# Kernel optimization log

Hardware: AMD Instinct MI355X
Metric: run time of the kernel (lower is better)

## Reference

```python
import jax, jax.numpy as jnp
import numpy as np

NEG_INF = -jnp.inf

def _sage_conv(x_src, x_dst, src, dst, Wl, bl, Wr, aggr, num_nodes):
    # messages = source features gathered along edges  [E, d]
    msgs = x_src[src]
    if aggr == 'mean':
        s = jax.ops.segment_sum(msgs, dst, num_segments=num_nodes)
        cnt = jax.ops.segment_sum(jnp.ones((src.shape[0],), x_src.dtype), dst, num_segments=num_nodes)
        agg = s / jnp.maximum(cnt, 1.0)[:, None]
    else:  # max; isolated targets -> 0 (PyG scatter-max fill)
        m = jax.ops.segment_max(msgs, dst, num_segments=num_nodes)
        agg = jnp.where(jnp.isfinite(m), m, 0.0)
    return agg @ Wl.T + bl + x_dst @ Wr.T

def setup_inputs() -> dict:
    key = jax.random.key(0)
    ks = jax.random.split(key, 12)
    N, E, D, H, C, L = 40000, 640000, 128, 128, 64, 2
    sc = 0.05
    return {
        'x': jax.random.normal(ks[0], (N, D), jnp.float32),
        'edge_index0': jax.random.randint(ks[1], (2, E), 0, N, jnp.int64),
        'edge_index1': jax.random.randint(ks[2], (2, E), 0, N, jnp.int64),
        'Wl_mean': jax.random.normal(ks[3], (L, H, D), jnp.float32) * sc,
        'bl_mean': jax.random.normal(ks[4], (L, H), jnp.float32) * sc,
        'Wr_mean': jax.random.normal(ks[5], (L, H, D), jnp.float32) * sc,
        'Wl_max': jax.random.normal(ks[6], (L, H, D), jnp.float32) * sc,
        'bl_max': jax.random.normal(ks[7], (L, H), jnp.float32) * sc,
        'Wr_max': jax.random.normal(ks[8], (L, H, D), jnp.float32) * sc,
        'post_W': jax.random.normal(ks[9], (C, 2 * L * H), jnp.float32) * sc,
        'post_b': jax.random.normal(ks[10], (C,), jnp.float32) * sc,
    }

def reference(x, edge_index0, edge_index1, Wl_mean, bl_mean, Wr_mean, Wl_max, bl_max, Wr_max, post_W, post_b):
    N = x.shape[0]
    edge_sets = [edge_index0, edge_index1]
    L = len(edge_sets)
    h = x
    all_layers = []
    for i, ei in enumerate(edge_sets):
        src, dst = ei[0], ei[1]
        x_mean = _sage_conv(h, h, src, dst, Wl_mean[i], bl_mean[i], Wr_mean[i], 'mean', N)
        x_max = _sage_conv(h, h, src, dst, Wl_max[i], bl_max[i], Wr_max[i], 'max', N)
        all_layers.append(x_mean)
        all_layers.append(x_max)
        if i != L - 1:
            h = jax.nn.relu(h)  # note: original never replaces x with conv output
    x_final = jnp.concatenate(all_layers, axis=1) @ post_W.T + post_b
    return jax.nn.log_softmax(x_final, axis=-1)
```

## Files before the change

### kernel.cpp

```cpp
#include <hip/hip_runtime.h>
#include <cstdint>
#include <cstddef>

constexpr int FD = 128;
constexpr int CC = 64;
constexpr int KTOT = 768;
constexpr int CAP = 48;
constexpr int EPT = 4;

typedef __attribute__((ext_vector_type(8))) short short8;
typedef __attribute__((ext_vector_type(4))) float f32x4;

__device__ __forceinline__ float bf2f(unsigned u16) {
  union { unsigned u; float f; } v; v.u = u16 << 16; return v.f;
}
__device__ __forceinline__ unsigned f2bf(float f) {
  union { float f; unsigned u; } v; v.f = f;
  return (v.u + 0x7FFFu + ((v.u >> 16) & 1u)) >> 16;
}
__device__ __forceinline__ unsigned pack2(float a, float b) {
  return f2bf(a) | (f2bf(b) << 16);
}
__device__ __forceinline__ unsigned relu_pk(unsigned v) {
  unsigned m = ((v >> 15) & 0x10001u) * 0xFFFFu;
  return v & ~m;
}

__global__ void init_kernel(const float* __restrict__ x, uint4* __restrict__ xbf4,
                            int n8, int* __restrict__ cnt, int ncnt) {
  int t = blockIdx.x * blockDim.x + threadIdx.x;
  if (t < ncnt) cnt[t] = 0;
  if (t >= n8) return;
  float4 a = *(const float4*)(x + (size_t)t * 8);
  float4 b = *(const float4*)(x + (size_t)t * 8 + 4);
  uint4 q;
  q.x = pack2(a.x, a.y); q.y = pack2(a.z, a.w);
  q.z = pack2(b.x, b.y); q.w = pack2(b.z, b.w);
  xbf4[t] = q;
}

__global__ void precompute_kernel(
    const float* __restrict__ Wl_mean, const float* __restrict__ bl_mean,
    const float* __restrict__ Wr_mean, const float* __restrict__ Wl_max,
    const float* __restrict__ bl_max,  const float* __restrict__ Wr_max,
    const float* __restrict__ postW,   const float* __restrict__ postb,
    unsigned short* __restrict__ Mbf, float* __restrict__ cb)
{
  int t = blockIdx.x * blockDim.x + threadIdx.x;
  if (t >= KTOT * CC) return;
  int c  = t & (CC - 1);
  int k  = t >> 6;
  int blk = k >> 7;
  int kk  = k & 127;
  const float* pw = postW + (size_t)c * 512;
  float acc = 0.f;
  if (blk < 4) {
    const float* W;
    if (blk == 0)      W = Wl_mean;
    else if (blk == 1) W = Wl_max;
    else if (blk == 2) W = Wl_mean + 128 * 128;
    else               W = Wl_max + 128 * 128;
    const float* p = pw + blk * 128;
    #pragma unroll 8
    for (int h = 0; h < 128; ++h) acc += p[h] * W[h * 128 + kk];
  } else if (blk == 4) {
    #pragma unroll 8
    for (int h = 0; h < 128; ++h)
      acc += pw[h] * Wr_mean[h * 128 + kk] + pw[128 + h] * Wr_max[h * 128 + kk];
  } else {
    const float* Wm = Wr_mean + 128 * 128;
    const float* Wx = Wr_max + 128 * 128;
    #pragma unroll 8
    for (int h = 0; h < 128; ++h)
      acc += pw[256 + h] * Wm[h * 128 + kk] + pw[384 + h] * Wx[h * 128 + kk];
  }
  Mbf[(size_t)c * KTOT + k] = (unsigned short)f2bf(acc);

  if (t < CC) {
    const float* pwc = postW + (size_t)t * 512;
    float b = postb[t];
    for (int h = 0; h < 128; ++h) {
      b += bl_mean[h]        * pwc[h]
         + bl_max[h]         * pwc[128 + h]
         + bl_mean[128 + h]  * pwc[256 + h]
         + bl_max[128 + h]   * pwc[384 + h];
    }
    cb[t] = b;
  }
}

__global__ __launch_bounds__(256) void build_kernel(
    const int* __restrict__ e0, int E0,
    const int* __restrict__ e1, int E1,
    int* __restrict__ cnt, unsigned short* __restrict__ csrf, int N)
{
  int t = blockIdx.x * blockDim.x + threadIdx.x;
  const int nt0 = (E0 + EPT - 1) / EPT;
  const int nt1 = (E1 + EPT - 1) / EPT;
  if (t >= nt0 + nt1) return;
  const int twoN = 2 * N;
  const int* e; int E; int cb2; int ti;
  if (t < nt0) { e = e0; E = E0; cb2 = 0; ti = t; }
  else         { e = e1; E = E1; cb2 = N; ti = t - nt0; }
  const int i0 = ti * EPT;

  if (i0 + EPT <= E) {
    int4 s4 = *(const int4*)(e + i0);
    int4 d4 = *(const int4*)(e + E + i0);
    int s[EPT] = {s4.x, s4.y, s4.z, s4.w};
    int d[EPT] = {d4.x, d4.y, d4.z, d4.w};
    int p[EPT];
    #pragma unroll
    for (int u = 0; u < EPT; ++u) p[u] = atomicAdd(&cnt[cb2 + d[u]], 1);
    #pragma unroll
    for (int u = 0; u < EPT; ++u)
      if (p[u] < CAP) csrf[(size_t)p[u] * twoN + cb2 + d[u]] = (unsigned short)s[u];
  } else {
    const int n = E - i0;
    for (int u = 0; u < n; ++u) {
      int ss = e[i0 + u], dd = e[E + i0 + u];
      int pp = atomicAdd(&cnt[cb2 + dd], 1);
      if (pp < CAP) csrf[(size_t)pp * twoN + cb2 + dd] = (unsigned short)ss;
    }
  }
}

__global__ __launch_bounds__(256) void agg_kernel(
    const unsigned* __restrict__ xbf, const int* __restrict__ cnt,
    const unsigned short* __restrict__ csrf, unsigned* __restrict__ aggbf, int N)
{
  int gw = (blockIdx.x * 256 + threadIdx.x) >> 6;
  int lane = threadIdx.x & 63;
  if (gw >= 2 * N) return;
  const int twoN = 2 * N;
  const int layer = (gw >= N) ? 1 : 0;
  const int node = gw - layer * N;
  const int deg = min(cnt[gw], CAP);
  const int half = lane >> 5;
  const int hl = lane & 31;
  const float lo = layer ? 0.f : -INFINITY;

  const int n0 = (deg + 1) >> 1;
  const int cbeg = half ? n0 : 0;
  const int ce = half ? deg : n0;

  float s0 = 0.f, s1 = 0.f, s2 = 0.f, s3 = 0.f;
  float m0 = -INFINITY, m1 = -INFINITY, m2 = -INFINITY, m3 = -INFINITY;

  for (int c = cbeg; c < ce; c += 8) {
    int idx[8];
    bool val[8];
    #pragma unroll
    for (int u = 0; u < 8; ++u) {
      int cc = c + u;
      val[u] = cc < ce;
      idx[u] = (int)csrf[(size_t)(val[u] ? cc : (ce - 1)) * twoN + gw];
    }
    uint2 g[8];
    #pragma unroll
    for (int u = 0; u < 8; ++u)
      g[u] = *(const uint2*)(xbf + (size_t)idx[u] * 64 + hl * 2);
    #pragma unroll
    for (int u = 0; u < 8; ++u) {
      float a0 = fmaxf(bf2f(g[u].x & 0xffffu), lo);
      float a1 = fmaxf(bf2f(g[u].x >> 16), lo);
      float a2 = fmaxf(bf2f(g[u].y & 0xffffu), lo);
      float a3 = fmaxf(bf2f(g[u].y >> 16), lo);
      s0 += val[u] ? a0 : 0.f;  s1 += val[u] ? a1 : 0.f;
      s2 += val[u] ? a2 : 0.f;  s3 += val[u] ? a3 : 0.f;
      m0 = fmaxf(m0, val[u] ? a0 : -INFINITY);
      m1 = fmaxf(m1, val[u] ? a1 : -INFINITY);
      m2 = fmaxf(m2, val[u] ? a2 : -INFINITY);
      m3 = fmaxf(m3, val[u] ? a3 : -INFINITY);
    }
  }

  s0 += __shfl_xor(s0, 32); s1 += __shfl_xor(s1, 32);
  s2 += __shfl_xor(s2, 32); s3 += __shfl_xor(s3, 32);
  m0 = fmaxf(m0, __shfl_xor(m0, 32)); m1 = fmaxf(m1, __shfl_xor(m1, 32));
  m2 = fmaxf(m2, __shfl_xor(m2, 32)); m3 = fmaxf(m3, __shfl_xor(m3, 32));

  if (half == 0) {
    float inv = 1.f / (float)(deg > 0 ? deg : 1);
    if (deg == 0) { m0 = 0.f; m1 = 0.f; m2 = 0.f; m3 = 0.f; }
    unsigned* am = aggbf + (size_t)(layer * 2)     * N * 64;
    unsigned* ax = aggbf + (size_t)(layer * 2 + 1) * N * 64;
    size_t o = (size_t)node * 64 + hl * 2;
    *(uint2*)(am + o) = make_uint2(pack2(s0 * inv, s1 * inv), pack2(s2 * inv, s3 * inv));
    *(uint2*)(ax + o) = make_uint2(pack2(m0, m1), pack2(m2, m3));
  }
}

__global__ __launch_bounds__(256) void gemm_kernel(
    const unsigned* __restrict__ aggbf, const unsigned* __restrict__ xbf,
    const unsigned short* __restrict__ Mbf, const float* __restrict__ cb,
    float* __restrict__ out, int N)
{
  const int tid = threadIdx.x;
  const int w = tid >> 6, l = tid & 63;
  const int l15 = l & 15, lg = l >> 4;
  const int rowb = blockIdx.x * 128 + w * 32;
  const int r0 = rowb + l15, r1 = r0 + 16;
  const size_t a0r = (size_t)min(r0, N - 1) * 64;
  const size_t a1r = (size_t)min(r1, N - 1) * 64;
  const int kg = lg * 8;
  const size_t N64 = (size_t)N * 64;

  f32x4 acc[2][4];
  #pragma unroll
  for (int i = 0; i < 2; ++i)
    #pragma unroll
    for (int j = 0; j < 4; ++j) acc[i][j] = (f32x4){0.f, 0.f, 0.f, 0.f};

  #pragma unroll
  for (int b6 = 0; b6 < 6; ++b6) {
    const unsigned* Ap = (b6 < 4) ? (aggbf + (size_t)b6 * N64) : xbf;
    #pragma unroll
    for (int ss = 0; ss < 4; ++ss) {
      const int k0 = b6 * 128 + ss * 32;
      const int ko = (ss * 32 + kg) >> 1;
      uint4 ua = *(const uint4*)(Ap + a0r + ko);
      uint4 ub = *(const uint4*)(Ap + a1r + ko);
      if (b6 == 5) {
        ua.x = relu_pk(ua.x); ua.y = relu_pk(ua.y);
        ua.z = relu_pk(ua.z); ua.w = relu_pk(ua.w);
        ub.x = relu_pk(ub.x); ub.y = relu_pk(ub.y);
        ub.z = relu_pk(ub.z); ub.w = relu_pk(ub.w);
      }
      short8 af0 = __builtin_bit_cast(short8, ua);
      short8 af1 = __builtin_bit_cast(short8, ub);
      #pragma unroll
      for (int fc = 0; fc < 4; ++fc) {
        const int c = fc * 16 + l15;
        uint4 qb = *(const uint4*)(Mbf + (size_t)c * KTOT + k0 + kg);
        short8 bf = __builtin_bit_cast(short8, qb);
        acc[0][fc] = __builtin_amdgcn_mfma_f32_16x16x32_bf16(af0, bf, acc[0][fc], 0, 0, 0);
        acc[1][fc] = __builtin_amdgcn_mfma_f32_16x16x32_bf16(af1, bf, acc[1][fc], 0, 0, 0);
      }
    }
  }

  float bias[4];
  #pragma unroll
  for (int fc = 0; fc < 4; ++fc) bias[fc] = cb[fc * 16 + l15];

  #pragma unroll
  for (int fr = 0; fr < 2; ++fr) {
    #pragma unroll
    for (int i = 0; i < 4; ++i) {
      int row = rowb + fr * 16 + lg * 4 + i;
      float z0 = acc[fr][0][i] + bias[0];
      float z1 = acc[fr][1][i] + bias[1];
      float z2 = acc[fr][2][i] + bias[2];
      float z3 = acc[fr][3][i] + bias[3];
      float m = fmaxf(fmaxf(z0, z1), fmaxf(z2, z3));
      #pragma unroll
      for (int o = 1; o < 16; o <<= 1) m = fmaxf(m, __shfl_xor(m, o));
      float s = expf(z0 - m) + expf(z1 - m) + expf(z2 - m) + expf(z3 - m);
      #pragma unroll
      for (int o = 1; o < 16; o <<= 1) s += __shfl_xor(s, o);
      float lse = m + logf(s);
      if (row < N) {
        size_t ob = (size_t)row * CC + l15;
        out[ob]      = z0 - lse;
        out[ob + 16] = z1 - lse;
        out[ob + 32] = z2 - lse;
        out[ob + 48] = z3 - lse;
      }
    }
  }
}

extern "C" void kernel_launch(void* const* d_in, const int* in_sizes, int n_in,
                              void* d_out, int out_size, void* d_ws, size_t ws_size,
                              hipStream_t stream)
{
  const float* x       = (const float*)d_in[0];
  const int*   e0      = (const int*)d_in[1];
  const int*   e1      = (const int*)d_in[2];
  const float* Wl_mean = (const float*)d_in[3];
  const float* bl_mean = (const float*)d_in[4];
  const float* Wr_mean = (const float*)d_in[5];
  const float* Wl_max  = (const float*)d_in[6];
  const float* bl_max  = (const float*)d_in[7];
  const float* Wr_max  = (const float*)d_in[8];
  const float* postW   = (const float*)d_in[9];
  const float* postb   = (const float*)d_in[10];
  float* out = (float*)d_out;

  const int N  = in_sizes[0] / FD;
  const int E0 = in_sizes[1] / 2;
  const int E1 = in_sizes[2] / 2;

  char* ws = (char*)d_ws;
  size_t off = 0;
  auto alloc = [&](size_t bytes) -> void* {
    void* p = ws + off;
    off = (off + bytes + 255) & ~(size_t)255;
    return p;
  };
  unsigned short* Mbf  = (unsigned short*)alloc((size_t)KTOT * CC * 2);
  float*          cbv  = (float*)alloc(CC * 4);
  int*            cnt  = (int*)alloc((size_t)2 * N * 4);
  unsigned short* csrf = (unsigned short*)alloc((size_t)2 * N * CAP * 2);
  unsigned*       xbf  = (unsigned*)alloc((size_t)N * 64 * 4);
  unsigned*       aggbf= (unsigned*)alloc((size_t)4 * N * 64 * 4);
  (void)ws_size; (void)n_in; (void)out_size;

  const int n8 = N * 16;
  init_kernel<<<dim3((n8 + 255) / 256), dim3(256), 0, stream>>>(
      x, (uint4*)xbf, n8, cnt, 2 * N);

  precompute_kernel<<<dim3((KTOT * CC + 255) / 256), dim3(256), 0, stream>>>(
      Wl_mean, bl_mean, Wr_mean, Wl_max, bl_max, Wr_max, postW, postb, Mbf, cbv);

  const int nthr = (E0 + EPT - 1) / EPT + (E1 + EPT - 1) / EPT;
  build_kernel<<<dim3((nthr + 255) / 256), dim3(256), 0, stream>>>(
      e0, E0, e1, E1, cnt, csrf, N);

  const int aggBlocks = (2 * N * 64 + 255) / 256;
  agg_kernel<<<dim3(aggBlocks), dim3(256), 0, stream>>>(xbf, cnt, csrf, aggbf, N);

  gemm_kernel<<<dim3((N + 127) / 128), dim3(256), 0, stream>>>(
      aggbf, xbf, Mbf, cbv, out, N);
}
```

Measured before the change: 277.6 us.

## Fuse all stages into one persistent cooperative kernel with grid syncs

Replaces the five separate launches (init, precompute, CSR build, aggregation, GEMM) with a single cooperative persistent kernel that runs grid-stride loops and uses grid.sync between phases. The GEMM phase also changes from 128-row tiles with two fragments per wave to 64-row tiles with one fragment per wave. The goal is to remove launch gaps and kernel-boundary overheads. The cost is grid-wide barriers, a grid capped by occupancy (at most 2048 blocks), less latency hiding in the gather-heavy aggregation, and possible register pressure from launch_bounds(256,4).

```diff
diff --git a/kernel.cpp b/kernel.cpp
--- a/kernel.cpp
+++ b/kernel.cpp
@@ -1,4 +1,5 @@
 #include <hip/hip_runtime.h>
+#include <hip/hip_cooperative_groups.h>
 #include <cstdint>
 #include <cstddef>
 
@@ -26,246 +27,246 @@
   return v & ~m;
 }
 
-__global__ void init_kernel(const float* __restrict__ x, uint4* __restrict__ xbf4,
-                            int n8, int* __restrict__ cnt, int ncnt) {
-  int t = blockIdx.x * blockDim.x + threadIdx.x;
-  if (t < ncnt) cnt[t] = 0;
-  if (t >= n8) return;
-  float4 a = *(const float4*)(x + (size_t)t * 8);
-  float4 b = *(const float4*)(x + (size_t)t * 8 + 4);
-  uint4 q;
-  q.x = pack2(a.x, a.y); q.y = pack2(a.z, a.w);
-  q.z = pack2(b.x, b.y); q.w = pack2(b.z, b.w);
-  xbf4[t] = q;
-}
-
-__global__ void precompute_kernel(
-    const float* __restrict__ Wl_mean, const float* __restrict__ bl_mean,
-    const float* __restrict__ Wr_mean, const float* __restrict__ Wl_max,
-    const float* __restrict__ bl_max,  const float* __restrict__ Wr_max,
-    const float* __restrict__ postW,   const float* __restrict__ postb,
-    unsigned short* __restrict__ Mbf, float* __restrict__ cb)
-{
-  int t = blockIdx.x * blockDim.x + threadIdx.x;
-  if (t >= KTOT * CC) return;
-  int c  = t & (CC - 1);
-  int k  = t >> 6;
-  int blk = k >> 7;
-  int kk  = k & 127;
-  const float* pw = postW + (size_t)c * 512;
-  float acc = 0.f;
-  if (blk < 4) {
-    const float* W;
-    if (blk == 0)      W = Wl_mean;
-    else if (blk == 1) W = Wl_max;
-    else if (blk == 2) W = Wl_mean + 128 * 128;
-    else               W = Wl_max + 128 * 128;
-    const float* p = pw + blk * 128;
-    #pragma unroll 8
-    for (int h = 0; h < 128; ++h) acc += p[h] * W[h * 128 + kk];
-  } else if (blk == 4) {
-    #pragma unroll 8
-    for (int h = 0; h < 128; ++h)
-      acc += pw[h] * Wr_mean[h * 128 + kk] + pw[128 + h] * Wr_max[h * 128 + kk];
-  } else {
-    const float* Wm = Wr_mean + 128 * 128;
-    const float* Wx = Wr_max + 128 * 128;
-    #pragma unroll 8
-    for (int h = 0; h < 128; ++h)
-      acc += pw[256 + h] * Wm[h * 128 + kk] + pw[384 + h] * Wx[h * 128 + kk];
-  }
-  Mbf[(size_t)c * KTOT + k] = (unsigned short)f2bf(acc);
-
-  if (t < CC) {
-    const float* pwc = postW + (size_t)t * 512;
-    float b = postb[t];
-    for (int h = 0; h < 128; ++h) {
-      b += bl_mean[h]        * pwc[h]
-         + bl_max[h]         * pwc[128 + h]
-         + bl_mean[128 + h]  * pwc[256 + h]
-         + bl_max[128 + h]   * pwc[384 + h];
-    }
-    cb[t] = b;
-  }
-}
-
-__global__ __launch_bounds__(256) void build_kernel(
-    const int* __restrict__ e0, int E0,
-    const int* __restrict__ e1, int E1,
-    int* __restrict__ cnt, unsigned short* __restrict__ csrf, int N)
-{
-  int t = blockIdx.x * blockDim.x + threadIdx.x;
-  const int nt0 = (E0 + EPT - 1) / EPT;
-  const int nt1 = (E1 + EPT - 1) / EPT;
-  if (t >= nt0 + nt1) return;
+struct MegaParams {
+  const float* x;
+  const int* e0;
+  const int* e1;
+  const float *Wl_mean, *bl_mean, *Wr_mean, *Wl_max, *bl_max, *Wr_max, *postW, *postb;
+  unsigned short* Mbf;
+  float* cb;
+  int* cnt;
+  unsigned short* csrf;
+  unsigned* xbf;
+  unsigned* aggbf;
+  float* out;
+  int N, E0, E1;
+};
+
+__global__ __launch_bounds__(256, 4) void mega_kernel(MegaParams p) {
+  cooperative_groups::grid_group grid = cooperative_groups::this_grid();
+  const int tid = threadIdx.x;
+  const int gtid = blockIdx.x * 256 + tid;
+  const int gsz = gridDim.x * 256;
+  const int N = p.N;
   const int twoN = 2 * N;
-  const int* e; int E; int cb2; int ti;
-  if (t < nt0) { e = e0; E = E0; cb2 = 0; ti = t; }
-  else         { e = e1; E = E1; cb2 = N; ti = t - nt0; }
-  const int i0 = ti * EPT;
-
-  if (i0 + EPT <= E) {
-    int4 s4 = *(const int4*)(e + i0);
-    int4 d4 = *(const int4*)(e + E + i0);
-    int s[EPT] = {s4.x, s4.y, s4.z, s4.w};
-    int d[EPT] = {d4.x, d4.y, d4.z, d4.w};
-    int p[EPT];
+
+  for (int t = gtid; t < twoN; t += gsz) p.cnt[t] = 0;
+
+  const int n8 = N * 16;
+  for (int t = gtid; t < n8; t += gsz) {
+    float4 a = *(const float4*)(p.x + (size_t)t * 8);
+    float4 b = *(const float4*)(p.x + (size_t)t * 8 + 4);
+    uint4 q;
+    q.x = pack2(a.x, a.y); q.y = pack2(a.z, a.w);
+    q.z = pack2(b.x, b.y); q.w = pack2(b.z, b.w);
+    ((uint4*)p.xbf)[t] = q;
+  }
+
+  for (int t = gtid; t < KTOT * CC; t += gsz) {
+    int c  = t & (CC - 1);
+    int k  = t >> 6;
+    int blk = k >> 7;
+    int kk  = k & 127;
+    const float* pw = p.postW + (size_t)c * 512;
+    float acc = 0.f;
+    if (blk < 4) {
+      const float* W;
+      if (blk == 0)      W = p.Wl_mean;
+      else if (blk == 1) W = p.Wl_max;
+      else if (blk == 2) W = p.Wl_mean + 128 * 128;
+      else               W = p.Wl_max + 128 * 128;
+      const float* pp = pw + blk * 128;
+      #pragma unroll 8
+      for (int h = 0; h < 128; ++h) acc += pp[h] * W[h * 128 + kk];
+    } else if (blk == 4) {
+      #pragma unroll 8
+      for (int h = 0; h < 128; ++h)
+        acc += pw[h] * p.Wr_mean[h * 128 + kk] + pw[128 + h] * p.Wr_max[h * 128 + kk];
+    } else {
+      const float* Wm = p.Wr_mean + 128 * 128;
+      const float* Wx = p.Wr_max + 128 * 128;
+      #pragma unroll 8
+      for (int h = 0; h < 128; ++h)
+        acc += pw[256 + h] * Wm[h * 128 + kk] + pw[384 + h] * Wx[h * 128 + kk];
+    }
+    p.Mbf[(size_t)c * KTOT + k] = (unsigned short)f2bf(acc);
+
+    if (t < CC) {
+      const float* pwc = p.postW + (size_t)t * 512;
+      float b = p.postb[t];
+      for (int h = 0; h < 128; ++h) {
+        b += p.bl_mean[h]       * pwc[h]
+           + p.bl_max[h]        * pwc[128 + h]
+           + p.bl_mean[128 + h] * pwc[256 + h]
+           + p.bl_max[128 + h]  * pwc[384 + h];
+      }
+      p.cb[t] = b;
+    }
+  }
+
+  grid.sync();
+
+  {
+    const int nt0 = (p.E0 + EPT - 1) / EPT;
+    const int nt1 = (p.E1 + EPT - 1) / EPT;
+    for (int u = gtid; u < nt0 + nt1; u += gsz) {
+      const int* e; int E; int cb2; int ti;
+      if (u < nt0) { e = p.e0; E = p.E0; cb2 = 0; ti = u; }
+      else         { e = p.e1; E = p.E1; cb2 = N; ti = u - nt0; }
+      const int i0 = ti * EPT;
+      if (i0 + EPT <= E) {
+        int4 s4 = *(const int4*)(e + i0);
+        int4 d4 = *(const int4*)(e + E + i0);
+        int s[EPT] = {s4.x, s4.y, s4.z, s4.w};
+        int d[EPT] = {d4.x, d4.y, d4.z, d4.w};
+        int pos[EPT];
+        #pragma unroll
+        for (int v = 0; v < EPT; ++v) pos[v] = atomicAdd(&p.cnt[cb2 + d[v]], 1);
+        #pragma unroll
+        for (int v = 0; v < EPT; ++v)
+          if (pos[v] < CAP) p.csrf[(size_t)pos[v] * twoN + cb2 + d[v]] = (unsigned short)s[v];
+      } else {
+        const int n = E - i0;
+        for (int v = 0; v < n; ++v) {
+          int ss = e[i0 + v], dd = e[E + i0 + v];
+          int pp2 = atomicAdd(&p.cnt[cb2 + dd], 1);
+          if (pp2 < CAP) p.csrf[(size_t)pp2 * twoN + cb2 + dd] = (unsigned short)ss;
+        }
+      }
+    }
+  }
+
+  grid.sync();
+
+  {
+    const int lane = tid & 63;
+    const int half = lane >> 5;
+    const int hl = lane & 31;
+    const int TW = gsz >> 6;
+    for (int gw = gtid >> 6; gw < twoN; gw += TW) {
+      const int layer = (gw >= N) ? 1 : 0;
+      const int node = gw - layer * N;
+      const int deg = min(p.cnt[gw], CAP);
+      const float lo = layer ? 0.f : -INFINITY;
+
+      const int n0 = (deg + 1) >> 1;
+      const int cbeg = half ? n0 : 0;
+      const int ce = half ? deg : n0;
+
+      float s0 = 0.f, s1 = 0.f, s2 = 0.f, s3 = 0.f;
+      float m0 = -INFINITY, m1 = -INFINITY, m2 = -INFINITY, m3 = -INFINITY;
+
+      for (int c = cbeg; c < ce; c += 8) {
+        int idx[8];
+        bool val[8];
+        #pragma unroll
+        for (int u = 0; u < 8; ++u) {
+          int cc = c + u;
+          val[u] = cc < ce;
+          idx[u] = (int)p.csrf[(size_t)(val[u] ? cc : (ce - 1)) * twoN + gw];
+        }
+        uint2 g[8];
+        #pragma unroll
+        for (int u = 0; u < 8; ++u)
+          g[u] = *(const uint2*)(p.xbf + (size_t)idx[u] * 64 + hl * 2);
+        #pragma unroll
+        for (int u = 0; u < 8; ++u) {
+          float a0 = fmaxf(bf2f(g[u].x & 0xffffu), lo);
+          float a1 = fmaxf(bf2f(g[u].x >> 16), lo);
+          float a2 = fmaxf(bf2f(g[u].y & 0xffffu), lo);
+          float a3 = fmaxf(bf2f(g[u].y >> 16), lo);
+          s0 += val[u] ? a0 : 0.f;  s1 += val[u] ? a1 : 0.f;
+          s2 += val[u] ? a2 : 0.f;  s3 += val[u] ? a3 : 0.f;
+          m0 = fmaxf(m0, val[u] ? a0 : -INFINITY);
+          m1 = fmaxf(m1, val[u] ? a1 : -INFINITY);
+          m2 = fmaxf(m2, val[u] ? a2 : -INFINITY);
+          m3 = fmaxf(m3, val[u] ? a3 : -INFINITY);
+        }
+      }
+
+      s0 += __shfl_xor(s0, 32); s1 += __shfl_xor(s1, 32);
+      s2 += __shfl_xor(s2, 32); s3 += __shfl_xor(s3, 32);
+      m0 = fmaxf(m0, __shfl_xor(m0, 32)); m1 = fmaxf(m1, __shfl_xor(m1, 32));
+      m2 = fmaxf(m2, __shfl_xor(m2, 32)); m3 = fmaxf(m3, __shfl_xor(m3, 32));
+
+      if (half == 0) {
+        float inv = 1.f / (float)(deg > 0 ? deg : 1);
+        if (deg == 0) { m0 = 0.f; m1 = 0.f; m2 = 0.f; m3 = 0.f; }
+        unsigned* am = p.aggbf + (size_t)(layer * 2)     * N * 64;
+        unsigned* ax = p.aggbf + (size_t)(layer * 2 + 1) * N * 64;
+        size_t o = (size_t)node * 64 + hl * 2;
+        *(uint2*)(am + o) = make_uint2(pack2(s0 * inv, s1 * inv), pack2(s2 * inv, s3 * inv));
+        *(uint2*)(ax + o) = make_uint2(pack2(m0, m1), pack2(m2, m3));
+      }
+    }
+  }
+
+  grid.sync();
+
+  {
+    const int w = tid >> 6, l = tid & 63;
+    const int l15 = l & 15, lg = l >> 4;
+    const int kg = lg * 8;
+    const size_t N64 = (size_t)N * 64;
+    const int ntiles = (N + 63) / 64;
+
+    float bias[4];
     #pragma unroll
-    for (int u = 0; u < EPT; ++u) p[u] = atomicAdd(&cnt[cb2 + d[u]], 1);
-    #pragma unroll
-    for (int u = 0; u < EPT; ++u)
-      if (p[u] < CAP) csrf[(size_t)p[u] * twoN + cb2 + d[u]] = (unsigned short)s[u];
-  } else {
-    const int n = E - i0;
-    for (int u = 0; u < n; ++u) {
-      int ss = e[i0 + u], dd = e[E + i0 + u];
-      int pp = atomicAdd(&cnt[cb2 + dd], 1);
-      if (pp < CAP) csrf[(size_t)pp * twoN + cb2 + dd] = (unsigned short)ss;
-    }
-  }
-}
-
-__global__ __launch_bounds__(256) void agg_kernel(
-    const unsigned* __restrict__ xbf, const int* __restrict__ cnt,
-    const unsigned short* __restrict__ csrf, unsigned* __restrict__ aggbf, int N)
-{
-  int gw = (blockIdx.x * 256 + threadIdx.x) >> 6;
-  int lane = threadIdx.x & 63;
-  if (gw >= 2 * N) return;
-  const int twoN = 2 * N;
-  const int layer = (gw >= N) ? 1 : 0;
-  const int node = gw - layer * N;
-  const int deg = min(cnt[gw], CAP);
-  const int half = lane >> 5;
-  const int hl = lane & 31;
-  const float lo = layer ? 0.f : -INFINITY;
-
-  const int n0 = (deg + 1) >> 1;
-  const int cbeg = half ? n0 : 0;
-  const int ce = half ? deg : n0;
-
-  float s0 = 0.f, s1 = 0.f, s2 = 0.f, s3 = 0.f;
-  float m0 = -INFINITY, m1 = -INFINITY, m2 = -INFINITY, m3 = -INFINITY;
-
-  for (int c = cbeg; c < ce; c += 8) {
-    int idx[8];
-    bool val[8];
-    #pragma unroll
-    for (int u = 0; u < 8; ++u) {
-      int cc = c + u;
-      val[u] = cc < ce;
-      idx[u] = (int)csrf[(size_t)(val[u] ? cc : (ce - 1)) * twoN + gw];
-    }
-    uint2 g[8];
-    #pragma unroll
-    for (int u = 0; u < 8; ++u)
-      g[u] = *(const uint2*)(xbf + (size_t)idx[u] * 64 + hl * 2);
-    #pragma unroll
-    for (int u = 0; u < 8; ++u) {
-      float a0 = fmaxf(bf2f(g[u].x & 0xffffu), lo);
-      float a1 = fmaxf(bf2f(g[u].x >> 16), lo);
-      float a2 = fmaxf(bf2f(g[u].y & 0xffffu), lo);
-      float a3 = fmaxf(bf2f(g[u].y >> 16), lo);
-      s0 += val[u] ? a0 : 0.f;  s1 += val[u] ? a1 : 0.f;
-      s2 += val[u] ? a2 : 0.f;  s3 += val[u] ? a3 : 0.f;
-      m0 = fmaxf(m0, val[u] ? a0 : -INFINITY);
-      m1 = fmaxf(m1, val[u] ? a1 : -INFINITY);
-      m2 = fmaxf(m2, val[u] ? a2 : -INFINITY);
-      m3 = fmaxf(m3, val[u] ? a3 : -INFINITY);
-    }
-  }
-
-  s0 += __shfl_xor(s0, 32); s1 += __shfl_xor(s1, 32);
-  s2 += __shfl_xor(s2, 32); s3 += __shfl_xor(s3, 32);
-  m0 = fmaxf(m0, __shfl_xor(m0, 32)); m1 = fmaxf(m1, __shfl_xor(m1, 32));
-  m2 = fmaxf(m2, __shfl_xor(m2, 32)); m3 = fmaxf(m3, __shfl_xor(m3, 32));
-
-  if (half == 0) {
-    float inv = 1.f / (float)(deg > 0 ? deg : 1);
-    if (deg == 0) { m0 = 0.f; m1 = 0.f; m2 = 0.f; m3 = 0.f; }
-    unsigned* am = aggbf + (size_t)(layer * 2)     * N * 64;
-    unsigned* ax = aggbf + (size_t)(layer * 2 + 1) * N * 64;
-    size_t o = (size_t)node * 64 + hl * 2;
-    *(uint2*)(am + o) = make_uint2(pack2(s0 * inv, s1 * inv), pack2(s2 * inv, s3 * inv));
-    *(uint2*)(ax + o) = make_uint2(pack2(m0, m1), pack2(m2, m3));
-  }
-}
-
-__global__ __launch_bounds__(256) void gemm_kernel(
-    const unsigned* __restrict__ aggbf, const unsigned* __restrict__ xbf,
-    const unsigned short* __restrict__ Mbf, const float* __restrict__ cb,
-    float* __restrict__ out, int N)
-{
-  const int tid = threadIdx.x;
-  const int w = tid >> 6, l = tid & 63;
-  const int l15 = l & 15, lg = l >> 4;
-  const int rowb = blockIdx.x * 128 + w * 32;
-  const int r0 = rowb + l15, r1 = r0 + 16;
-  const size_t a0r = (size_t)min(r0, N - 1) * 64;
-  const size_t a1r = (size_t)min(r1, N - 1) * 64;
-  const int kg = lg * 8;
-  const size_t N64 = (size_t)N * 64;
-
-  f32x4 acc[2][4];
-  #pragma unroll
-  for (int i = 0; i < 2; ++i)
-    #pragma unroll
-    for (int j = 0; j < 4; ++j) acc[i][j] = (f32x4){0.f, 0.f, 0.f, 0.f};
-
-  #pragma unroll
-  for (int b6 = 0; b6 < 6; ++b6) {
-    const unsigned* Ap = (b6 < 4) ? (aggbf + (size_t)b6 * N64) : xbf;
-    #pragma unroll
-    for (int ss = 0; ss < 4; ++ss) {
-      const int k0 = b6 * 128 + ss * 32;
-      const int ko = (ss * 32 + kg) >> 1;
-      uint4 ua = *(const uint4*)(Ap + a0r + ko);
-      uint4 ub = *(const uint4*)(Ap + a1r + ko);
-      if (b6 == 5) {
-        ua.x = relu_pk(ua.x); ua.y = relu_pk(ua.y);
-        ua.z = relu_pk(ua.z); ua.w = relu_pk(ua.w);
-        ub.x = relu_pk(ub.x); ub.y = relu_pk(ub.y);
-        ub.z = relu_pk(ub.z); ub.w = relu_pk(ub.w);
-      }
-      short8 af0 = __builtin_bit_cast(short8, ua);
-      short8 af1 = __builtin_bit_cast(short8, ub);
+    for (int fc = 0; fc < 4; ++fc) bias[fc] = p.cb[fc * 16 + l15];
+
+    for (int t = blockIdx.x; t < ntiles; t += gridDim.x) {
+      const int rowb = t * 64 + w * 16;
+      const int r0 = rowb + l15;
+      const size_t a0r = (size_t)min(r0, N - 1) * 64;
+
+      f32x4 acc[4];
       #pragma unroll
-      for (int fc = 0; fc < 4; ++fc) {
-        const int c = fc * 16 + l15;
-        uint4 qb = *(const uint4*)(Mbf + (size_t)c * KTOT + k0 + kg);
-        short8 bf = __builtin_bit_cast(short8, qb);
-        acc[0][fc] = __builtin_amdgcn_mfma_f32_16x16x32_bf16(af0, bf, acc[0][fc], 0, 0, 0);
-        acc[1][fc] = __builtin_amdgcn_mfma_f32_16x16x32_bf16(af1, bf, acc[1][fc], 0, 0, 0);
-      }
-    }
-  }
-
-  float bias[4];
-  #pragma unroll
-  for (int fc = 0; fc < 4; ++fc) bias[fc] = cb[fc * 16 + l15];
-
-  #pragma unroll
-  for (int fr = 0; fr < 2; ++fr) {
-    #pragma unroll
-    for (int i = 0; i < 4; ++i) {
-      int row = rowb + fr * 16 + lg * 4 + i;
-      float z0 = acc[fr][0][i] + bias[0];
-      float z1 = acc[fr][1][i] + bias[1];
-      float z2 = acc[fr][2][i] + bias[2];
-      float z3 = acc[fr][3][i] + bias[3];
-      float m = fmaxf(fmaxf(z0, z1), fmaxf(z2, z3));
+      for (int j = 0; j < 4; ++j) acc[j] = (f32x4){0.f, 0.f, 0.f, 0.f};
+
       #pragma unroll
-      for (int o = 1; o < 16; o <<= 1) m = fmaxf(m, __shfl_xor(m, o));
-      float s = expf(z0 - m) + expf(z1 - m) + expf(z2 - m) + expf(z3 - m);
+      for (int b6 = 0; b6 < 6; ++b6) {
+        const unsigned* Ap = (b6 < 4) ? (p.aggbf + (size_t)b6 * N64) : p.xbf;
+        #pragma unroll
+        for (int ss = 0; ss < 4; ++ss) {
+          const int k0 = b6 * 128 + ss * 32;
+          const int ko = (ss * 32 + kg) >> 1;
+          uint4 ua = *(const uint4*)(Ap + a0r + ko);
+          if (b6 == 5) {
+            ua.x = relu_pk(ua.x); ua.y = relu_pk(ua.y);
+            ua.z = relu_pk(ua.z); ua.w = relu_pk(ua.w);
+          }
+          short8 af = __builtin_bit_cast(short8, ua);
+          #pragma unroll
+          for (int fc = 0; fc < 4; ++fc) {
+            const int c = fc * 16 + l15;
+            uint4 qb = *(const uint4*)(p.Mbf + (size_t)c * KTOT + k0 + kg);
+            short8 bf = __builtin_bit_cast(short8, qb);
+            acc[fc] = __builtin_amdgcn_mfma_f32_16x16x32_bf16(af, bf, acc[fc], 0, 0, 0);
+          }
+        }
+      }
+
       #pragma unroll
-      for (int o = 1; o < 16; o <<= 1) s += __shfl_xor(s, o);
-      float lse = m + logf(s);
-      if (row < N) {
-        size_t ob = (size_t)row * CC + l15;
-        out[ob]      = z0 - lse;
-        out[ob + 16] = z1 - lse;
-        out[ob + 32] = z2 - lse;
-        out[ob + 48] = z3 - lse;
+      for (int i = 0; i < 4; ++i) {
+        int row = rowb + lg * 4 + i;
+        float z0 = acc[0][i] + bias[0];
+        float z1 = acc[1][i] + bias[1];
+        float z2 = acc[2][i] + bias[2];
+        float z3 = acc[3][i] + bias[3];
+        float m = fmaxf(fmaxf(z0, z1), fmaxf(z2, z3));
+        #pragma unroll
+        for (int o = 1; o < 16; o <<= 1) m = fmaxf(m, __shfl_xor(m, o));
+        float s = expf(z0 - m) + expf(z1 - m) + expf(z2 - m) + expf(z3 - m);
+        #pragma unroll
+        for (int o = 1; o < 16; o <<= 1) s += __shfl_xor(s, o);
+        float lse = m + logf(s);
+        if (row < N) {
+          size_t ob = (size_t)row * CC + l15;
+          p.out[ob]      = z0 - lse;
+          p.out[ob + 16] = z1 - lse;
+          p.out[ob + 32] = z2 - lse;
+          p.out[ob + 48] = z3 - lse;
+        }
       }
     }
   }
@@ -275,52 +276,47 @@
                               void* d_out, int out_size, void* d_ws, size_t ws_size,
                               hipStream_t stream)
 {
-  const float* x       = (const float*)d_in[0];
-  const int*   e0      = (const int*)d_in[1];
-  const int*   e1      = (const int*)d_in[2];
-  const float* Wl_mean = (const float*)d_in[3];
-  const float* bl_mean = (const float*)d_in[4];
-  const float* Wr_mean = (const float*)d_in[5];
-  const float* Wl_max  = (const float*)d_in[6];
-  const float* bl_max  = (const float*)d_in[7];
-  const float* Wr_max  = (const float*)d_in[8];
-  const float* postW   = (const float*)d_in[9];
-  const float* postb   = (const float*)d_in[10];
-  float* out = (float*)d_out;
-
-  const int N  = in_sizes[0] / FD;
-  const int E0 = in_sizes[1] / 2;
-  const int E1 = in_sizes[2] / 2;
+  MegaParams p;
+  p.x       = (const float*)d_in[0];
+  p.e0      = (const int*)d_in[1];
+  p.e1      = (const int*)d_in[2];
+  p.Wl_mean = (const float*)d_in[3];
+  p.bl_mean = (const float*)d_in[4];
+  p.Wr_mean = (const float*)d_in[5];
+  p.Wl_max  = (const float*)d_in[6];
+  p.bl_max  = (const float*)d_in[7];
+  p.Wr_max  = (const float*)d_in[8];
+  p.postW   = (const float*)d_in[9];
+  p.postb   = (const float*)d_in[10];
+  p.out     = (float*)d_out;
+
+  p.N  = in_sizes[0] / FD;
+  p.E0 = in_sizes[1] / 2;
+  p.E1 = in_sizes[2] / 2;
+  const int N = p.N;
 
   char* ws = (char*)d_ws;
   size_t off = 0;
   auto alloc = [&](size_t bytes) -> void* {
-    void* p = ws + off;
+    void* pp = ws + off;
     off = (off + bytes + 255) & ~(size_t)255;
-    return p;
+    return pp;
   };
-  unsigned short* Mbf  = (unsigned short*)alloc((size_t)KTOT * CC * 2);
-  float*          cbv  = (float*)alloc(CC * 4);
-  int*            cnt  = (int*)alloc((size_t)2 * N * 4);
-  unsigned short* csrf = (unsigned short*)alloc((size_t)2 * N * CAP * 2);
-  unsigned*       xbf  = (unsigned*)alloc((size_t)N * 64 * 4);
-  unsigned*       aggbf= (unsigned*)alloc((size_t)4 * N * 64 * 4);
+  p.Mbf   = (unsigned short*)alloc((size_t)KTOT * CC * 2);
+  p.cb    = (float*)alloc(CC * 4);
+  p.cnt   = (int*)alloc((size_t)2 * N * 4);
+  p.csrf  = (unsigned short*)alloc((size_t)2 * N * CAP * 2);
+  p.xbf   = (unsigned*)alloc((size_t)N * 64 * 4);
+  p.aggbf = (unsigned*)alloc((size_t)4 * N * 64 * 4);
   (void)ws_size; (void)n_in; (void)out_size;
 
-  const int n8 = N * 16;
-  init_kernel<<<dim3((n8 + 255) / 256), dim3(256), 0, stream>>>(
-      x, (uint4*)xbf, n8, cnt, 2 * N);
-
-  precompute_kernel<<<dim3((KTOT * CC + 255) / 256), dim3(256), 0, stream>>>(
-      Wl_mean, bl_mean, Wr_mean, Wl_max, bl_max, Wr_max, postW, postb, Mbf, cbv);
-
-  const int nthr = (E0 + EPT - 1) / EPT + (E1 + EPT - 1) / EPT;
-  build_kernel<<<dim3((nthr + 255) / 256), dim3(256), 0, stream>>>(
-      e0, E0, e1, E1, cnt, csrf, N);
-
-  const int aggBlocks = (2 * N * 64 + 255) / 256;
-  agg_kernel<<<dim3(aggBlocks), dim3(256), 0, stream>>>(xbf, cnt, csrf, aggbf, N);
-
-  gemm_kernel<<<dim3((N + 127) / 128), dim3(256), 0, stream>>>(
-      aggbf, xbf, Mbf, cbv, out, N);
-}
+  int occ = 0;
+  hipError_t err = hipOccupancyMaxActiveBlocksPerMultiprocessor(
+      &occ, mega_kernel, 256, 0);
+  if (err != hipSuccess || occ < 1) occ = 2;
+  int G = occ * 256;
+  if (G > 2048) G = 2048;
+
+  void* args[] = {(void*)&p};
+  hipLaunchCooperativeKernel((void*)mega_kernel, dim3(G), dim3(256), args, 0, stream);
+}
```

Measured after the change: 509.5 us. 1.83x slower.
